# Performance work log

Measured on AMD Instinct MI355X. Metric: run time of the kernel, lower is better.

## Reference

```python
import jax, jax.numpy as jnp
import numpy as np

D_MODEL = 1024
N_HEAD = 16
D_K = D_MODEL // N_HEAD


def setup_inputs() -> dict:
    key = jax.random.key(0)
    ks = jax.random.split(key, 11)
    B, T = 2, 2048
    s = 1.0 / np.sqrt(D_MODEL)
    return {
        "q": jax.random.normal(ks[0], (B, T, D_MODEL), jnp.float32),
        "k": jax.random.normal(ks[1], (B, T, D_MODEL), jnp.float32),
        "v": jax.random.normal(ks[2], (B, T, D_MODEL), jnp.float32),
        "w_q": jax.random.normal(ks[3], (D_MODEL, D_MODEL), jnp.float32) * s,
        "b_q": jax.random.normal(ks[4], (D_MODEL,), jnp.float32) * 0.01,
        "w_k": jax.random.normal(ks[5], (D_MODEL, D_MODEL), jnp.float32) * s,
        "b_k": jax.random.normal(ks[6], (D_MODEL,), jnp.float32) * 0.01,
        "w_v": jax.random.normal(ks[7], (D_MODEL, D_MODEL), jnp.float32) * s,
        "b_v": jax.random.normal(ks[8], (D_MODEL,), jnp.float32) * 0.01,
        "w_o": jax.random.normal(ks[9], (D_MODEL, D_MODEL), jnp.float32) * s,
        "b_o": jax.random.normal(ks[10], (D_MODEL,), jnp.float32) * 0.01,
    }


def reference(q, k, v, w_q, b_q, w_k, b_k, w_v, b_v, w_o, b_o):
    B, T, _ = q.shape
    # QKV projections -> [B, H, T, d_k]
    def proj(x, w, b):
        return (jnp.einsum('btd,de->bte', x, w) + b).reshape(B, T, N_HEAD, D_K).transpose(0, 2, 1, 3)
    qh = proj(q, w_q, b_q)
    kh = proj(k, w_k, b_k)
    vh = proj(v, w_v, b_v)
    scale = jnp.float32(1.0 / np.sqrt(D_K))
    scores = jnp.einsum('bhqd,bhkd->bhqk', qh, kh) * scale  # [B,H,T,T]
    attn = jax.nn.softmax(scores, axis=-1)
    # dropout is identity in eval mode
    out = jnp.einsum('bhqk,bhkd->bhqd', attn, vh)  # [B,H,T,d_k]
    out = out.transpose(0, 2, 1, 3).reshape(B, T, N_HEAD * D_K)
    return jnp.einsum('btd,de->bte', out, w_o) + b_o
```

## Files before the change

### kernel.cpp

```cpp
#include <hip/hip_runtime.h>
#include <stdint.h>

#define DEVI static __device__ __forceinline__

typedef float f32x4 __attribute__((ext_vector_type(4)));
typedef float f32x16 __attribute__((ext_vector_type(16)));
typedef short s16x8 __attribute__((ext_vector_type(8)));
typedef unsigned short u16x4 __attribute__((ext_vector_type(4)));
typedef uint32_t u32x2 __attribute__((ext_vector_type(2)));
typedef uint32_t u32x4 __attribute__((ext_vector_type(4)));

DEVI unsigned short f2bf(float f) {
  union { float f; uint32_t u; } v; v.f = f;
  uint32_t u = v.u;
  return (unsigned short)((u + 0x7fffu + ((u >> 16) & 1u)) >> 16);
}

DEVI float bf2f(unsigned short u) {
  union { uint32_t u; float f; } v;
  v.u = ((uint32_t)u) << 16;
  return v.f;
}

DEVI uint32_t cvtpk(float lo, float hi) {
  uint32_t r;
  asm("v_cvt_pk_bf16_f32 %0, %1, %2" : "=v"(r) : "v"(lo), "v"(hi));
  return r;
}

DEVI float fexp2(float x) {
#if __has_builtin(__builtin_amdgcn_exp2f)
  return __builtin_amdgcn_exp2f(x);
#else
  return exp2f(x);
#endif
}

DEVI float max3(float a, float b, float c) {
  float r;
  asm("v_max3_f32 %0, %1, %2, %3" : "=v"(r) : "v"(a), "v"(b), "v"(c));
  return r;
}

DEVI void pl32swap(uint32_t& a, uint32_t& b) {
#if __has_builtin(__builtin_amdgcn_permlane32_swap)
  u32x2 r = __builtin_amdgcn_permlane32_swap(a, b, false, false);
  a = r[0]; b = r[1];
#else
  asm("v_permlane32_swap_b32 %0, %1" : "+v"(a), "+v"(b));
#endif
}

DEVI float swap_half(float x, int hi) {
  uint32_t a = __float_as_uint(x), b = a;
  pl32swap(a, b);
  return hi ? __uint_as_float(a) : __uint_as_float(b);
}

DEVI void g2l16(const void* g, void* l) {
  __builtin_amdgcn_global_load_lds(
      (const __attribute__((address_space(1))) void*)g,
      (__attribute__((address_space(3))) void*)l, 16, 0, 0);
}

DEVI float vmax16(const f32x16& v) {
  float a = max3(v[0], v[1], v[2]);
  float b = max3(v[3], v[4], v[5]);
  float c = max3(v[6], v[7], v[8]);
  float d = max3(v[9], v[10], v[11]);
  float e = max3(v[12], v[13], v[14]);
  float x = max3(a, b, c);
  float y = max3(d, e, v[15]);
  return fmaxf(x, y);
}

DEVI float vsum16(const f32x16& v) {
  float a = (v[0] + v[1]) + (v[2] + v[3]);
  float b = (v[4] + v[5]) + (v[6] + v[7]);
  float c = (v[8] + v[9]) + (v[10] + v[11]);
  float d = (v[12] + v[13]) + (v[14] + v[15]);
  return (a + b) + (c + d);
}

__global__ __launch_bounds__(256) void k_prep(
    const float* __restrict__ q, const float* __restrict__ k,
    const float* __restrict__ v, unsigned short* __restrict__ qkv,
    const float* __restrict__ w0, const float* __restrict__ w1,
    const float* __restrict__ w2, const float* __restrict__ w3,
    unsigned short* __restrict__ t0, unsigned short* __restrict__ t1,
    unsigned short* __restrict__ t2, unsigned short* __restrict__ t3) {
  __shared__ float tile[32][33];
  const int bx = blockIdx.x;
  if (bx < 3072) {
    const int y = bx >> 10;
    const float* in = y == 0 ? q : y == 1 ? k : v;
    unsigned short* o = qkv + (size_t)y * 4194304;
    int idx = (bx & 1023) * 256 + threadIdx.x;
    for (int i = idx * 4; i < 4194304; i += 1048576) {
      f32x4 x = *(const f32x4*)(in + i);
      u16x4 r;
      for (int j = 0; j < 4; ++j) r[j] = f2bf(x[j]);
      *(u16x4*)(o + i) = r;
    }
  } else {
    const int wb = bx - 3072;
    const int z = wb >> 10, tb = wb & 1023;
    const float* w = z == 0 ? w0 : z == 1 ? w1 : z == 2 ? w2 : w3;
    unsigned short* wt = z == 0 ? t0 : z == 1 ? t1 : z == 2 ? t2 : t3;
    const int n0 = (tb & 31) * 32, k0 = (tb >> 5) * 32;
    const int tx = threadIdx.x & 31, ty = threadIdx.x >> 5;
    for (int j = 0; j < 4; ++j)
      tile[ty + j * 8][tx] = w[(size_t)(k0 + ty + j * 8) * 1024 + n0 + tx];
    __syncthreads();
    for (int j = 0; j < 4; ++j)
      wt[(size_t)(n0 + ty + j * 8) * 1024 + k0 + tx] = f2bf(tile[tx][ty + j * 8]);
  }
}

__global__ __launch_bounds__(256) void k_gemm_multi(
    const unsigned short* A0, const unsigned short* A1, const unsigned short* A2,
    const unsigned short* B0, const unsigned short* B1, const unsigned short* B2,
    const float* c0, const float* c1, const float* c2,
    void* o0, void* o1, void* o2, int mode0) {
  constexpr int K = 1024;
  const int z = blockIdx.y;
  const unsigned short* A = z == 0 ? A0 : z == 1 ? A1 : A2;
  const unsigned short* Bt = z == 0 ? B0 : z == 1 ? B1 : B2;
  const float* bias = z == 0 ? c0 : z == 1 ? c1 : c2;
  void* outp = z == 0 ? o0 : z == 1 ? o1 : o2;
  const int MODE = mode0 + z;

  __shared__ __align__(16) unsigned short As[128 * 64];
  __shared__ __align__(16) unsigned short Bs[64 * 64];
  const int tid = threadIdx.x;
  const int lane = tid & 63, w = tid >> 6;
  const int g = lane >> 4, c = lane & 15;
  const int wgid = (blockIdx.x & 7) * 64 + (blockIdx.x >> 3);
  const int bm = wgid >> 4, bn = wgid & 15;
  const int m0 = bm * 128, n0 = bn * 64;
  const int wr = w >> 1, wc = w & 1;
  f32x4 acc[4][2] = {};

  for (int kt = 0; kt < 16; ++kt) {
    const int k0 = kt * 64;
    __syncthreads();
#pragma unroll
    for (int it = 0; it < 4; ++it) {
      int e = it * 256 + tid;
      int row = e >> 3, cwp = (e & 7) ^ (row & 7);
      g2l16(A + (size_t)(m0 + row) * K + k0 + cwp * 8,
            (char*)As + (it * 256 + (w << 6)) * 16);
    }
#pragma unroll
    for (int it = 0; it < 2; ++it) {
      int e = it * 256 + tid;
      int row = e >> 3, cwp = (e & 7) ^ (row & 7);
      g2l16(Bt + (size_t)(n0 + row) * K + k0 + cwp * 8,
            (char*)Bs + (it * 256 + (w << 6)) * 16);
    }
    __syncthreads();
    for (int kk = 0; kk < 2; ++kk) {
      s16x8 af[4], bfr[2];
      for (int mi = 0; mi < 4; ++mi) {
        int row = wr * 64 + mi * 16 + c;
        int ch = (kk * 4 + g) ^ (row & 7);
        af[mi] = *(const s16x8*)((const char*)As + row * 128 + ch * 16);
      }
      for (int ni = 0; ni < 2; ++ni) {
        int row = wc * 32 + ni * 16 + c;
        int ch = (kk * 4 + g) ^ (row & 7);
        bfr[ni] = *(const s16x8*)((const char*)Bs + row * 128 + ch * 16);
      }
      for (int mi = 0; mi < 4; ++mi)
        for (int ni = 0; ni < 2; ++ni)
          acc[mi][ni] = __builtin_amdgcn_mfma_f32_16x16x32_bf16(
              af[mi], bfr[ni], acc[mi][ni], 0, 0, 0);
    }
  }

  if (MODE == 0 || MODE == 1) {
    unsigned short* out = (unsigned short*)outp;
    const float scale = (MODE == 0) ? 0.1803368801111204f : 1.0f;
    for (int mi = 0; mi < 4; ++mi)
      for (int ni = 0; ni < 2; ++ni) {
        int row = m0 + wr * 64 + mi * 16 + g * 4;
        int col = n0 + wc * 32 + ni * 16 + c;
        float bb = bias[col];
        for (int r = 0; r < 4; ++r)
          out[(size_t)(row + r) * 1024 + col] = f2bf((acc[mi][ni][r] + bb) * scale);
      }
  } else if (MODE == 2) {
    unsigned short* vt = (unsigned short*)outp;
    const int bq = m0 >> 11, t0 = m0 & 2047;
    for (int mi = 0; mi < 4; ++mi)
      for (int ni = 0; ni < 2; ++ni) {
        int rowb = wr * 64 + mi * 16 + g * 4;
        int coll = wc * 32 + ni * 16 + c;
        float bb = bias[n0 + coll];
        u16x4 pk;
        for (int r = 0; r < 4; ++r) pk[r] = f2bf(acc[mi][ni][r] + bb);
        *(u16x4*)(vt + (size_t)(bq * 1024 + n0 + coll) * 2048 + t0 + rowb) = pk;
      }
  } else {
    float* out = (float*)outp;
    for (int mi = 0; mi < 4; ++mi)
      for (int ni = 0; ni < 2; ++ni) {
        int row = m0 + wr * 64 + mi * 16 + g * 4;
        int col = n0 + wc * 32 + ni * 16 + c;
        float bb = bias[col];
        for (int r = 0; r < 4; ++r)
          out[(size_t)(row + r) * 1024 + col] = acc[mi][ni][r] + bb;
      }
  }
}

__global__ __launch_bounds__(256) void k_attn(const unsigned short* __restrict__ Qp,
                                              const unsigned short* __restrict__ Kp,
                                              const unsigned short* __restrict__ Vt,
                                              unsigned short* __restrict__ Po0,
                                              unsigned short* __restrict__ Po1,
                                              unsigned short* __restrict__ Po2,
                                              unsigned short* __restrict__ Po3,
                                              float2* __restrict__ ml) {
  __shared__ __align__(16) unsigned short Ks[2][4096];
  __shared__ __align__(16) unsigned short Vs[2][4096];
  const int tid = threadIdx.x;
  const int lane = tid & 63, w = tid >> 6;
  const int l31 = lane & 31, hi = lane >> 5;
  const int blk = (blockIdx.x & 7) * 256 + (blockIdx.x >> 3);
  const int sp = blk & 3, qt = (blk >> 2) & 15, bh = blk >> 6;
  const int b = bh >> 4, h = bh & 15;
  const int m0 = qt * 128 + w * 32;
  const size_t qkBase = (size_t)b * 2048 * 1024 + (size_t)h * 64;
  const size_t vtBase = ((size_t)b * 1024 + h * 64) * 2048;

  const unsigned short* qrow = Qp + qkBase + (size_t)(m0 + l31) * 1024;
  s16x8 bq[4];
#pragma unroll
  for (int s = 0; s < 4; ++s)
    bq[s] = *(const s16x8*)(qrow + s * 16 + hi * 8);

  const int srow = tid >> 2, c4 = tid & 3;
  const unsigned short* kg = Kp + qkBase + (size_t)srow * 1024 + c4 * 16 +
                             (size_t)sp * 524288;
  const unsigned short* vg = Vt + vtBase + (size_t)srow * 2048 + c4 * 16 +
                             sp * 512;
  int wof[2];
#pragma unroll
  for (int j = 0; j < 2; ++j)
    wof[j] = srow * 128 + (((c4 * 2 + j) ^ (srow & 7)) * 16);

  float m_run = -1e30f, l_run = 0.f;
  f32x16 o0 = {}, o1 = {};

  {
    s16x8 k0 = *(const s16x8*)(kg), k1 = *(const s16x8*)(kg + 8);
    s16x8 v0 = *(const s16x8*)(vg), v1 = *(const s16x8*)(vg + 8);
    *(s16x8*)((char*)&Ks[0][0] + wof[0]) = k0;
    *(s16x8*)((char*)&Ks[0][0] + wof[1]) = k1;
    *(s16x8*)((char*)&Vs[0][0] + wof[0]) = v0;
    *(s16x8*)((char*)&Vs[0][0] + wof[1]) = v1;
  }
  __syncthreads();

  const int rch = l31 & 7;

#pragma unroll 1
  for (int t = 0; t < 8; ++t) {
    const int cur = t & 1;
    s16x8 k0, k1, v0, v1;
    if (t < 7) {
      const unsigned short* kgt = kg + (size_t)(t + 1) * 65536;
      const unsigned short* vgt = vg + (t + 1) * 64;
      k0 = *(const s16x8*)(kgt); k1 = *(const s16x8*)(kgt + 8);
      v0 = *(const s16x8*)(vgt); v1 = *(const s16x8*)(vgt + 8);
    }
    const char* ks = (const char*)&Ks[cur][0];
    const char* vs = (const char*)&Vs[cur][0];

    f32x16 s0 = {}, s1 = {};
    __builtin_amdgcn_s_setprio(1);
#pragma unroll
    for (int ds = 0; ds < 4; ++ds) {
      int ch = (2 * ds + hi) ^ rch;
      s16x8 a0 = *(const s16x8*)(ks + l31 * 128 + ch * 16);
      s16x8 a1 = *(const s16x8*)(ks + (32 + l31) * 128 + ch * 16);
      s0 = __builtin_amdgcn_mfma_f32_32x32x16_bf16(a0, bq[ds], s0, 0, 0, 0);
      s1 = __builtin_amdgcn_mfma_f32_32x32x16_bf16(a1, bq[ds], s1, 0, 0, 0);
    }
    __builtin_amdgcn_s_setprio(0);

    float tm = fmaxf(vmax16(s0), vmax16(s1));
    tm = fmaxf(tm, swap_half(tm, hi));
    if (!__all(tm - m_run <= 8.0f)) {
      float mt = fmaxf(m_run, tm);
      float al = fexp2(m_run - mt);
      l_run *= al;
#pragma unroll
      for (int j = 0; j < 16; ++j) { o0[j] *= al; o1[j] *= al; }
      m_run = mt;
    }
#pragma unroll
    for (int j = 0; j < 16; ++j) s0[j] = fexp2(s0[j] - m_run);
#pragma unroll
    for (int j = 0; j < 16; ++j) s1[j] = fexp2(s1[j] - m_run);
    l_run += vsum16(s0) + vsum16(s1);

    s16x8 pf[4];
    {
      uint32_t w0 = cvtpk(s0[0], s0[1]), w1 = cvtpk(s0[2], s0[3]);
      uint32_t w2 = cvtpk(s0[4], s0[5]), w3 = cvtpk(s0[6], s0[7]);
      uint32_t w4 = cvtpk(s0[8], s0[9]), w5 = cvtpk(s0[10], s0[11]);
      uint32_t w6 = cvtpk(s0[12], s0[13]), w7 = cvtpk(s0[14], s0[15]);
      pl32swap(w0, w2); pl32swap(w1, w3); pl32swap(w4, w6); pl32swap(w5, w7);
      u32x4 f0 = {w0, w1, w2, w3}, f1 = {w4, w5, w6, w7};
      pf[0] = *(s16x8*)&f0;
      pf[1] = *(s16x8*)&f1;
    }
    {
      uint32_t w0 = cvtpk(s1[0], s1[1]), w1 = cvtpk(s1[2], s1[3]);
      uint32_t w2 = cvtpk(s1[4], s1[5]), w3 = cvtpk(s1[6], s1[7]);
      uint32_t w4 = cvtpk(s1[8], s1[9]), w5 = cvtpk(s1[10], s1[11]);
      uint32_t w6 = cvtpk(s1[12], s1[13]), w7 = cvtpk(s1[14], s1[15]);
      pl32swap(w0, w2); pl32swap(w1, w3); pl32swap(w4, w6); pl32swap(w5, w7);
      u32x4 f0 = {w0, w1, w2, w3}, f1 = {w4, w5, w6, w7};
      pf[2] = *(s16x8*)&f0;
      pf[3] = *(s16x8*)&f1;
    }

    __builtin_amdgcn_s_setprio(1);
#pragma unroll
    for (int ksp = 0; ksp < 4; ++ksp) {
      int ch = (2 * ksp + hi) ^ rch;
      s16x8 a0 = *(const s16x8*)(vs + l31 * 128 + ch * 16);
      s16x8 a1 = *(const s16x8*)(vs + (32 + l31) * 128 + ch * 16);
      o0 = __builtin_amdgcn_mfma_f32_32x32x16_bf16(a0, pf[ksp], o0, 0, 0, 0);
      o1 = __builtin_amdgcn_mfma_f32_32x32x16_bf16(a1, pf[ksp], o1, 0, 0, 0);
    }
    __builtin_amdgcn_s_setprio(0);

    if (t < 7) {
      const int nb = cur ^ 1;
      *(s16x8*)((char*)&Ks[nb][0] + wof[0]) = k0;
      *(s16x8*)((char*)&Ks[nb][0] + wof[1]) = k1;
      *(s16x8*)((char*)&Vs[nb][0] + wof[0]) = v0;
      *(s16x8*)((char*)&Vs[nb][0] + wof[1]) = v1;
    }
    __syncthreads();
  }

  float lt = l_run + swap_half(l_run, hi);
  float inv = 1.0f / lt;
  unsigned short* Po = sp == 0 ? Po0 : sp == 1 ? Po1 : sp == 2 ? Po2 : Po3;
  unsigned short* arow = Po + ((size_t)b * 2048 + m0 + l31) * 1024 + h * 64;
#pragma unroll
  for (int dblk = 0; dblk < 2; ++dblk) {
#pragma unroll
    for (int rq = 0; rq < 4; ++rq) {
      float e0 = (dblk ? o1[rq * 4 + 0] : o0[rq * 4 + 0]) * inv;
      float e1 = (dblk ? o1[rq * 4 + 1] : o0[rq * 4 + 1]) * inv;
      float e2 = (dblk ? o1[rq * 4 + 2] : o0[rq * 4 + 2]) * inv;
      float e3 = (dblk ? o1[rq * 4 + 3] : o0[rq * 4 + 3]) * inv;
      u32x2 pk;
      pk[0] = cvtpk(e0, e1);
      pk[1] = cvtpk(e2, e3);
      *(u32x2*)(arow + dblk * 32 + 8 * rq + 4 * hi) = pk;
    }
  }
  if (hi == 0) {
    int qid = ((b << 4) + h) * 2048 + m0 + l31;
    ml[sp * 65536 + qid] = {m_run, lt};
  }
}

__global__ __launch_bounds__(256) void k_comb(const unsigned short* __restrict__ Po0,
                                              const unsigned short* __restrict__ Po1,
                                              const unsigned short* __restrict__ Po2,
                                              const unsigned short* __restrict__ Po3,
                                              const float2* __restrict__ ml,
                                              unsigned short* __restrict__ Att) {
  int idx = blockIdx.x * 256 + threadIdx.x;
  int base = idx * 8;
  int qrow = base >> 10, col = base & 1023;
  int h = col >> 6, b = qrow >> 11, t = qrow & 2047;
  int qid = ((b << 4) + h) * 2048 + t;
  float2 p0 = ml[qid], p1 = ml[65536 + qid];
  float2 p2 = ml[131072 + qid], p3 = ml[196608 + qid];
  float ms = fmaxf(fmaxf(p0.x, p1.x), fmaxf(p2.x, p3.x));
  float a0 = fexp2(p0.x - ms) * p0.y, a1 = fexp2(p1.x - ms) * p1.y;
  float a2 = fexp2(p2.x - ms) * p2.y, a3 = fexp2(p3.x - ms) * p3.y;
  float inv = 1.0f / ((a0 + a1) + (a2 + a3));
  float w0 = a0 * inv, w1 = a1 * inv, w2 = a2 * inv, w3 = a3 * inv;
  s16x8 v0 = *(const s16x8*)(Po0 + base);
  s16x8 v1 = *(const s16x8*)(Po1 + base);
  s16x8 v2 = *(const s16x8*)(Po2 + base);
  s16x8 v3 = *(const s16x8*)(Po3 + base);
  u32x4 pk;
#pragma unroll
  for (int j = 0; j < 4; ++j) {
    float e0 = w0 * bf2f((unsigned short)v0[2 * j]) + w1 * bf2f((unsigned short)v1[2 * j]) +
               w2 * bf2f((unsigned short)v2[2 * j]) + w3 * bf2f((unsigned short)v3[2 * j]);
    float e1 = w0 * bf2f((unsigned short)v0[2 * j + 1]) + w1 * bf2f((unsigned short)v1[2 * j + 1]) +
               w2 * bf2f((unsigned short)v2[2 * j + 1]) + w3 * bf2f((unsigned short)v3[2 * j + 1]);
    pk[j] = cvtpk(e0, e1);
  }
  *(u32x4*)(Att + base) = pk;
}

extern "C" void kernel_launch(void* const* d_in, const int* in_sizes, int n_in,
                              void* d_out, int out_size, void* d_ws, size_t ws_size,
                              hipStream_t stream) {
  const float* q = (const float*)d_in[0];
  const float* k = (const float*)d_in[1];
  const float* v = (const float*)d_in[2];
  const float* w_q = (const float*)d_in[3];
  const float* b_q = (const float*)d_in[4];
  const float* w_k = (const float*)d_in[5];
  const float* b_k = (const float*)d_in[6];
  const float* w_v = (const float*)d_in[7];
  const float* b_v = (const float*)d_in[8];
  const float* w_o = (const float*)d_in[9];
  const float* b_o = (const float*)d_in[10];

  unsigned short* s = (unsigned short*)d_ws;
  unsigned short* qbf = s;
  unsigned short* kbf = s + 4194304;
  unsigned short* vbf = s + 8388608;
  unsigned short* wqT = s + 12582912;
  unsigned short* wkT = s + 13631488;
  unsigned short* wvT = s + 14680064;
  unsigned short* woT = s + 15728640;
  unsigned short* Qp  = s + 16777216;
  unsigned short* Kp  = s + 20971520;
  unsigned short* Vt  = s + 25165824;
  unsigned short* Po3 = s + 29360128;
  unsigned short* Po0 = qbf;
  unsigned short* Po1 = kbf;
  unsigned short* Po2 = vbf;
  unsigned short* Att = Qp;
  float2* ml = (float2*)wqT;

  k_prep<<<7168, 256, 0, stream>>>(q, k, v, qbf, w_q, w_k, w_v, w_o,
                                   wqT, wkT, wvT, woT);

  k_gemm_multi<<<dim3(512, 3), 256, 0, stream>>>(
      qbf, kbf, vbf, wqT, wkT, wvT, b_q, b_k, b_v,
      (void*)Qp, (void*)Kp, (void*)Vt, 0);

  k_attn<<<2048, 256, 0, stream>>>(Qp, Kp, Vt, Po0, Po1, Po2, Po3, ml);

  k_comb<<<2048, 256, 0, stream>>>(Po0, Po1, Po2, Po3, ml, Att);

  k_gemm_multi<<<dim3(512, 1), 256, 0, stream>>>(
      Att, Att, Att, woT, woT, woT, b_o, b_o, b_o,
      d_out, d_out, d_out, 3);
}
```

Before: 137.5 us.

## Halve attention KV splits and software-pipeline PV MFMA behind next QK

Attention now splits the key range into 2 halves instead of 4, so each block runs 16 tiles and the combine kernel reads two partial outputs instead of four. The loop is restructured so the PV MFMAs for the previous tile run right after the QK MFMAs of the current tile, with V triple-buffered in shared memory, letting softmax work overlap matrix-core work. This cuts partial-output traffic and combine work, at the cost of half as many blocks (1024) and so less parallelism. It also adds LDS and register pressure from the extra V buffer and the live P fragments.

```diff
diff --git a/kernel.cpp b/kernel.cpp
--- a/kernel.cpp
+++ b/kernel.cpp
@@ -80,6 +80,45 @@
   float c = (v[8] + v[9]) + (v[10] + v[11]);
   float d = (v[12] + v[13]) + (v[14] + v[15]);
   return (a + b) + (c + d);
+}
+
+DEVI void sm_group(f32x16& s0, f32x16& s1, float& m_run, float& l_run,
+                   f32x16& o0, f32x16& o1, int hi, s16x8 (&pf)[4]) {
+  float tm = fmaxf(vmax16(s0), vmax16(s1));
+  tm = fmaxf(tm, swap_half(tm, hi));
+  if (!__all(tm - m_run <= 8.0f)) {
+    float mt = fmaxf(m_run, tm);
+    float al = fexp2(m_run - mt);
+    l_run *= al;
+#pragma unroll
+    for (int j = 0; j < 16; ++j) { o0[j] *= al; o1[j] *= al; }
+    m_run = mt;
+  }
+#pragma unroll
+  for (int j = 0; j < 16; ++j) s0[j] = fexp2(s0[j] - m_run);
+#pragma unroll
+  for (int j = 0; j < 16; ++j) s1[j] = fexp2(s1[j] - m_run);
+  l_run += vsum16(s0) + vsum16(s1);
+  {
+    uint32_t w0 = cvtpk(s0[0], s0[1]), w1 = cvtpk(s0[2], s0[3]);
+    uint32_t w2 = cvtpk(s0[4], s0[5]), w3 = cvtpk(s0[6], s0[7]);
+    uint32_t w4 = cvtpk(s0[8], s0[9]), w5 = cvtpk(s0[10], s0[11]);
+    uint32_t w6 = cvtpk(s0[12], s0[13]), w7 = cvtpk(s0[14], s0[15]);
+    pl32swap(w0, w2); pl32swap(w1, w3); pl32swap(w4, w6); pl32swap(w5, w7);
+    u32x4 f0 = {w0, w1, w2, w3}, f1 = {w4, w5, w6, w7};
+    pf[0] = *(s16x8*)&f0;
+    pf[1] = *(s16x8*)&f1;
+  }
+  {
+    uint32_t w0 = cvtpk(s1[0], s1[1]), w1 = cvtpk(s1[2], s1[3]);
+    uint32_t w2 = cvtpk(s1[4], s1[5]), w3 = cvtpk(s1[6], s1[7]);
+    uint32_t w4 = cvtpk(s1[8], s1[9]), w5 = cvtpk(s1[10], s1[11]);
+    uint32_t w6 = cvtpk(s1[12], s1[13]), w7 = cvtpk(s1[14], s1[15]);
+    pl32swap(w0, w2); pl32swap(w1, w3); pl32swap(w4, w6); pl32swap(w5, w7);
+    u32x4 f0 = {w0, w1, w2, w3}, f1 = {w4, w5, w6, w7};
+    pf[2] = *(s16x8*)&f0;
+    pf[3] = *(s16x8*)&f1;
+  }
 }
 
 __global__ __launch_bounds__(256) void k_prep(
@@ -219,16 +258,14 @@
                                               const unsigned short* __restrict__ Vt,
                                               unsigned short* __restrict__ Po0,
                                               unsigned short* __restrict__ Po1,
-                                              unsigned short* __restrict__ Po2,
-                                              unsigned short* __restrict__ Po3,
                                               float2* __restrict__ ml) {
   __shared__ __align__(16) unsigned short Ks[2][4096];
-  __shared__ __align__(16) unsigned short Vs[2][4096];
+  __shared__ __align__(16) unsigned short Vs[3][4096];
   const int tid = threadIdx.x;
   const int lane = tid & 63, w = tid >> 6;
   const int l31 = lane & 31, hi = lane >> 5;
-  const int blk = (blockIdx.x & 7) * 256 + (blockIdx.x >> 3);
-  const int sp = blk & 3, qt = (blk >> 2) & 15, bh = blk >> 6;
+  const int blk = (blockIdx.x & 7) * 128 + (blockIdx.x >> 3);
+  const int half = blk & 1, qt = (blk >> 1) & 15, bh = blk >> 5;
   const int b = bh >> 4, h = bh & 15;
   const int m0 = qt * 128 + w * 32;
   const size_t qkBase = (size_t)b * 2048 * 1024 + (size_t)h * 64;
@@ -242,9 +279,9 @@
 
   const int srow = tid >> 2, c4 = tid & 3;
   const unsigned short* kg = Kp + qkBase + (size_t)srow * 1024 + c4 * 16 +
-                             (size_t)sp * 524288;
+                             (size_t)half * 1048576;
   const unsigned short* vg = Vt + vtBase + (size_t)srow * 2048 + c4 * 16 +
-                             sp * 512;
+                             half * 1024;
   int wof[2];
 #pragma unroll
   for (int j = 0; j < 2; ++j)
@@ -252,6 +289,7 @@
 
   float m_run = -1e30f, l_run = 0.f;
   f32x16 o0 = {}, o1 = {};
+  s16x8 pf[4];
 
   {
     s16x8 k0 = *(const s16x8*)(kg), k1 = *(const s16x8*)(kg + 8);
@@ -264,19 +302,19 @@
   __syncthreads();
 
   const int rch = l31 & 7;
+  int vr = 2, vw = 1;
 
 #pragma unroll 1
-  for (int t = 0; t < 8; ++t) {
-    const int cur = t & 1;
-    s16x8 k0, k1, v0, v1;
-    if (t < 7) {
+  for (int t = 0; t < 16; ++t) {
+    const int kcur = t & 1;
+    s16x8 k0r, k1r, v0r, v1r;
+    if (t < 15) {
       const unsigned short* kgt = kg + (size_t)(t + 1) * 65536;
       const unsigned short* vgt = vg + (t + 1) * 64;
-      k0 = *(const s16x8*)(kgt); k1 = *(const s16x8*)(kgt + 8);
-      v0 = *(const s16x8*)(vgt); v1 = *(const s16x8*)(vgt + 8);
-    }
-    const char* ks = (const char*)&Ks[cur][0];
-    const char* vs = (const char*)&Vs[cur][0];
+      k0r = *(const s16x8*)(kgt); k1r = *(const s16x8*)(kgt + 8);
+      v0r = *(const s16x8*)(vgt); v1r = *(const s16x8*)(vgt + 8);
+    }
+    const char* ks = (const char*)&Ks[kcur][0];
 
     f32x16 s0 = {}, s1 = {};
     __builtin_amdgcn_s_setprio(1);
@@ -288,46 +326,34 @@
       s0 = __builtin_amdgcn_mfma_f32_32x32x16_bf16(a0, bq[ds], s0, 0, 0, 0);
       s1 = __builtin_amdgcn_mfma_f32_32x32x16_bf16(a1, bq[ds], s1, 0, 0, 0);
     }
+    if (t > 0) {
+      const char* vs = (const char*)&Vs[vr][0];
+#pragma unroll
+      for (int ksp = 0; ksp < 4; ++ksp) {
+        int ch = (2 * ksp + hi) ^ rch;
+        s16x8 a0 = *(const s16x8*)(vs + l31 * 128 + ch * 16);
+        s16x8 a1 = *(const s16x8*)(vs + (32 + l31) * 128 + ch * 16);
+        o0 = __builtin_amdgcn_mfma_f32_32x32x16_bf16(a0, pf[ksp], o0, 0, 0, 0);
+        o1 = __builtin_amdgcn_mfma_f32_32x32x16_bf16(a1, pf[ksp], o1, 0, 0, 0);
+      }
+    }
     __builtin_amdgcn_s_setprio(0);
 
-    float tm = fmaxf(vmax16(s0), vmax16(s1));
-    tm = fmaxf(tm, swap_half(tm, hi));
-    if (!__all(tm - m_run <= 8.0f)) {
-      float mt = fmaxf(m_run, tm);
-      float al = fexp2(m_run - mt);
-      l_run *= al;
-#pragma unroll
-      for (int j = 0; j < 16; ++j) { o0[j] *= al; o1[j] *= al; }
-      m_run = mt;
-    }
-#pragma unroll
-    for (int j = 0; j < 16; ++j) s0[j] = fexp2(s0[j] - m_run);
-#pragma unroll
-    for (int j = 0; j < 16; ++j) s1[j] = fexp2(s1[j] - m_run);
-    l_run += vsum16(s0) + vsum16(s1);
-
-    s16x8 pf[4];
-    {
-      uint32_t w0 = cvtpk(s0[0], s0[1]), w1 = cvtpk(s0[2], s0[3]);
-      uint32_t w2 = cvtpk(s0[4], s0[5]), w3 = cvtpk(s0[6], s0[7]);
-      uint32_t w4 = cvtpk(s0[8], s0[9]), w5 = cvtpk(s0[10], s0[11]);
-      uint32_t w6 = cvtpk(s0[12], s0[13]), w7 = cvtpk(s0[14], s0[15]);
-      pl32swap(w0, w2); pl32swap(w1, w3); pl32swap(w4, w6); pl32swap(w5, w7);
-      u32x4 f0 = {w0, w1, w2, w3}, f1 = {w4, w5, w6, w7};
-      pf[0] = *(s16x8*)&f0;
-      pf[1] = *(s16x8*)&f1;
-    }
-    {
-      uint32_t w0 = cvtpk(s1[0], s1[1]), w1 = cvtpk(s1[2], s1[3]);
-      uint32_t w2 = cvtpk(s1[4], s1[5]), w3 = cvtpk(s1[6], s1[7]);
-      uint32_t w4 = cvtpk(s1[8], s1[9]), w5 = cvtpk(s1[10], s1[11]);
-      uint32_t w6 = cvtpk(s1[12], s1[13]), w7 = cvtpk(s1[14], s1[15]);
-      pl32swap(w0, w2); pl32swap(w1, w3); pl32swap(w4, w6); pl32swap(w5, w7);
-      u32x4 f0 = {w0, w1, w2, w3}, f1 = {w4, w5, w6, w7};
-      pf[2] = *(s16x8*)&f0;
-      pf[3] = *(s16x8*)&f1;
-    }
-
+    sm_group(s0, s1, m_run, l_run, o0, o1, hi, pf);
+
+    if (t < 15) {
+      *(s16x8*)((char*)&Ks[kcur ^ 1][0] + wof[0]) = k0r;
+      *(s16x8*)((char*)&Ks[kcur ^ 1][0] + wof[1]) = k1r;
+      *(s16x8*)((char*)&Vs[vw][0] + wof[0]) = v0r;
+      *(s16x8*)((char*)&Vs[vw][0] + wof[1]) = v1r;
+    }
+    __syncthreads();
+    vr = vr == 2 ? 0 : vr + 1;
+    vw = vw == 2 ? 0 : vw + 1;
+  }
+
+  {
+    const char* vs = (const char*)&Vs[vr][0];
     __builtin_amdgcn_s_setprio(1);
 #pragma unroll
     for (int ksp = 0; ksp < 4; ++ksp) {
@@ -338,20 +364,11 @@
       o1 = __builtin_amdgcn_mfma_f32_32x32x16_bf16(a1, pf[ksp], o1, 0, 0, 0);
     }
     __builtin_amdgcn_s_setprio(0);
-
-    if (t < 7) {
-      const int nb = cur ^ 1;
-      *(s16x8*)((char*)&Ks[nb][0] + wof[0]) = k0;
-      *(s16x8*)((char*)&Ks[nb][0] + wof[1]) = k1;
-      *(s16x8*)((char*)&Vs[nb][0] + wof[0]) = v0;
-      *(s16x8*)((char*)&Vs[nb][0] + wof[1]) = v1;
-    }
-    __syncthreads();
   }
 
   float lt = l_run + swap_half(l_run, hi);
   float inv = 1.0f / lt;
-  unsigned short* Po = sp == 0 ? Po0 : sp == 1 ? Po1 : sp == 2 ? Po2 : Po3;
+  unsigned short* Po = half ? Po1 : Po0;
   unsigned short* arow = Po + ((size_t)b * 2048 + m0 + l31) * 1024 + h * 64;
 #pragma unroll
   for (int dblk = 0; dblk < 2; ++dblk) {
@@ -369,14 +386,12 @@
   }
   if (hi == 0) {
     int qid = ((b << 4) + h) * 2048 + m0 + l31;
-    ml[sp * 65536 + qid] = {m_run, lt};
+    ml[half * 65536 + qid] = {m_run, lt};
   }
 }
 
 __global__ __launch_bounds__(256) void k_comb(const unsigned short* __restrict__ Po0,
                                               const unsigned short* __restrict__ Po1,
-                                              const unsigned short* __restrict__ Po2,
-                                              const unsigned short* __restrict__ Po3,
                                               const float2* __restrict__ ml,
                                               unsigned short* __restrict__ Att) {
   int idx = blockIdx.x * 256 + threadIdx.x;
@@ -385,23 +400,17 @@
   int h = col >> 6, b = qrow >> 11, t = qrow & 2047;
   int qid = ((b << 4) + h) * 2048 + t;
   float2 p0 = ml[qid], p1 = ml[65536 + qid];
-  float2 p2 = ml[131072 + qid], p3 = ml[196608 + qid];
-  float ms = fmaxf(fmaxf(p0.x, p1.x), fmaxf(p2.x, p3.x));
+  float ms = fmaxf(p0.x, p1.x);
   float a0 = fexp2(p0.x - ms) * p0.y, a1 = fexp2(p1.x - ms) * p1.y;
-  float a2 = fexp2(p2.x - ms) * p2.y, a3 = fexp2(p3.x - ms) * p3.y;
-  float inv = 1.0f / ((a0 + a1) + (a2 + a3));
-  float w0 = a0 * inv, w1 = a1 * inv, w2 = a2 * inv, w3 = a3 * inv;
+  float inv = 1.0f / (a0 + a1);
+  float w0 = a0 * inv, w1 = a1 * inv;
   s16x8 v0 = *(const s16x8*)(Po0 + base);
   s16x8 v1 = *(const s16x8*)(Po1 + base);
-  s16x8 v2 = *(const s16x8*)(Po2 + base);
-  s16x8 v3 = *(const s16x8*)(Po3 + base);
   u32x4 pk;
 #pragma unroll
   for (int j = 0; j < 4; ++j) {
-    float e0 = w0 * bf2f((unsigned short)v0[2 * j]) + w1 * bf2f((unsigned short)v1[2 * j]) +
-               w2 * bf2f((unsigned short)v2[2 * j]) + w3 * bf2f((unsigned short)v3[2 * j]);
-    float e1 = w0 * bf2f((unsigned short)v0[2 * j + 1]) + w1 * bf2f((unsigned short)v1[2 * j + 1]) +
-               w2 * bf2f((unsigned short)v2[2 * j + 1]) + w3 * bf2f((unsigned short)v3[2 * j + 1]);
+    float e0 = w0 * bf2f((unsigned short)v0[2 * j]) + w1 * bf2f((unsigned short)v1[2 * j]);
+    float e1 = w0 * bf2f((unsigned short)v0[2 * j + 1]) + w1 * bf2f((unsigned short)v1[2 * j + 1]);
     pk[j] = cvtpk(e0, e1);
   }
   *(u32x4*)(Att + base) = pk;
@@ -433,11 +442,9 @@
   unsigned short* Qp  = s + 16777216;
   unsigned short* Kp  = s + 20971520;
   unsigned short* Vt  = s + 25165824;
-  unsigned short* Po3 = s + 29360128;
   unsigned short* Po0 = qbf;
   unsigned short* Po1 = kbf;
-  unsigned short* Po2 = vbf;
-  unsigned short* Att = Qp;
+  unsigned short* Att = vbf;
   float2* ml = (float2*)wqT;
 
   k_prep<<<7168, 256, 0, stream>>>(q, k, v, qbf, w_q, w_k, w_v, w_o,
@@ -447,9 +454,9 @@
       qbf, kbf, vbf, wqT, wkT, wvT, b_q, b_k, b_v,
       (void*)Qp, (void*)Kp, (void*)Vt, 0);
 
-  k_attn<<<2048, 256, 0, stream>>>(Qp, Kp, Vt, Po0, Po1, Po2, Po3, ml);
-
-  k_comb<<<2048, 256, 0, stream>>>(Po0, Po1, Po2, Po3, ml, Att);
+  k_attn<<<1024, 256, 0, stream>>>(Qp, Kp, Vt, Po0, Po1, ml);
+
+  k_comb<<<2048, 256, 0, stream>>>(Po0, Po1, ml, Att);
 
   k_gemm_multi<<<dim3(512, 1), 256, 0, stream>>>(
       Att, Att, Att, woT, woT, woT, b_o, b_o, b_o,
```

After: 130.4 us. -5.2%, faster.
